# Performance work log

Measured on AMD Instinct MI355X. Metric: run time of the kernel, lower is better.

Reference implementation:

```python
import jax, jax.numpy as jnp
import numpy as np

N_DIM = 512
HEADS = 8
NUM_EXPERTS = 65536
NUM_KEYS = 256      # sqrt(NUM_EXPERTS)
DIM_KEY = 256       # N_DIM // 2
TOPK = 16           # num_experts_per_head (also product_key_topk)
SCALE = 0.02


def setup_inputs() -> dict:
    key = jax.random.key(0)
    k0, k1, k2, k3, k4 = jax.random.split(key, 5)
    x = jax.random.normal(k0, (1, 2048, N_DIM), dtype=jnp.float32)
    W_q = jax.random.normal(k1, (N_DIM, 2 * HEADS * DIM_KEY), dtype=jnp.float32) * SCALE
    keys = jax.random.normal(k2, (HEADS, NUM_KEYS, 2, DIM_KEY), dtype=jnp.float32) * SCALE
    down_embed = jax.random.normal(k3, (NUM_EXPERTS, N_DIM), dtype=jnp.float32) * SCALE
    up_embed = jax.random.normal(k4, (NUM_EXPERTS, N_DIM), dtype=jnp.float32) * SCALE
    return {"x": x, "W_q": W_q, "keys": keys, "down_embed": down_embed, "up_embed": up_embed}


def reference(x, W_q, keys, down_embed, up_embed):
    b, n, d = x.shape
    # queries: [b,n,2*h*dk] -> [2,b,n,h,dk]
    q = (x @ W_q).reshape(b, n, 2, HEADS, DIM_KEY).transpose(2, 0, 1, 3, 4)
    # similarity against product keys: [2,b,n,h,num_keys]
    sim = jnp.einsum('pbnhd,hkpd->pbnhk', q, keys)
    sx, ix = jax.lax.top_k(sim[0], TOPK)   # [b,n,h,TOPK]
    sy, iy = jax.lax.top_k(sim[1], TOPK)
    # cartesian product of the two top-k sets -> [b,n,h,TOPK*TOPK]
    all_scores = (sx[..., :, None] + sy[..., None, :]).reshape(b, n, HEADS, TOPK * TOPK)
    scores, pk_idx = jax.lax.top_k(all_scores, TOPK)  # [b,n,h,TOPK]
    # NOTE: original module indexes embeddings with pk_idx (flat top-k positions),
    # reproduced faithfully here.
    w_down = down_embed[pk_idx]  # [b,n,h,TOPK,d]
    w_up = up_embed[pk_idx]      # [b,n,h,TOPK,d]
    h = jnp.einsum('bnd,bnhkd->bnhk', x, w_down)
    h = jax.nn.gelu(h, approximate=False)
    h = jax.nn.softmax(scores, axis=-1) * h
    return jnp.einsum('bnhk,bnhkd->bnd', h, w_up)
```

## Files before the change

kernel.cpp:

```cpp
#include <hip/hip_runtime.h>
#include <math.h>

#define N_TOK 2048
#define NDIM 512
#define HEADS 8
#define TOPK 16
#define QCOLS 4096
#define LSC 4096.0f
#define ILSC (1.0f/4096.0f)

typedef __attribute__((ext_vector_type(8))) _Float16 f16x8;
typedef __attribute__((ext_vector_type(4))) float f32x4;

__device__ __forceinline__ unsigned short f32_to_f16(float f) {
    _Float16 h = (_Float16)f;
    return __builtin_bit_cast(unsigned short, h);
}
__device__ __forceinline__ float f16_to_f32(unsigned short u) {
    return (float)__builtin_bit_cast(_Float16, u);
}
__device__ __forceinline__ void gl_lds16(const void* g, void* l) {
    __builtin_amdgcn_global_load_lds(
        (const __attribute__((address_space(1))) void*)g,
        (__attribute__((address_space(3))) void*)l, 16, 0, 0);
}

__device__ __forceinline__ void split_f4(const float* __restrict__ src,
                                         unsigned short* __restrict__ dh,
                                         unsigned short* __restrict__ dl,
                                         int i) {
    float4 v = reinterpret_cast<const float4*>(src)[i];
    float vv[4] = {v.x, v.y, v.z, v.w};
    ushort4 h, lo;
    unsigned short* hp = &h.x; unsigned short* lp = &lo.x;
    #pragma unroll
    for (int q = 0; q < 4; ++q) {
        unsigned short hh = f32_to_f16(vv[q]);
        hp[q] = hh;
        lp[q] = f32_to_f16((vv[q] - f16_to_f32(hh)) * LSC);
    }
    reinterpret_cast<ushort4*>(dh)[i] = h;
    reinterpret_cast<ushort4*>(dl)[i] = lo;
}

__global__ __launch_bounds__(256) void kP_split(const float* __restrict__ x,
                                                const float* __restrict__ Wq,
                                                const float* __restrict__ keys,
                                                const float* __restrict__ down,
                                                const float* __restrict__ up,
                                                unsigned short* __restrict__ xh,
                                                unsigned short* __restrict__ xl,
                                                unsigned short* __restrict__ Wqh,
                                                unsigned short* __restrict__ Wql,
                                                unsigned short* __restrict__ ksh,
                                                unsigned short* __restrict__ ksl,
                                                unsigned short* __restrict__ Mth,
                                                unsigned short* __restrict__ Mtl,
                                                unsigned short* __restrict__ upTh,
                                                unsigned short* __restrict__ upTl) {
    const int bid = blockIdx.x;
    const int tid = threadIdx.x;
    if (bid < 256) {
        #pragma unroll
        for (int t = 0; t < 4; ++t) split_f4(x, xh, xl, bid * 1024 + t * 256 + tid);
        return;
    }
    if (bid < 768) {
        const int b = bid - 256;
        #pragma unroll
        for (int t = 0; t < 4; ++t) split_f4(Wq, Wqh, Wql, b * 1024 + t * 256 + tid);
        return;
    }
    if (bid < 1024) {
        const int b = bid - 768;
        #pragma unroll
        for (int t = 0; t < 4; ++t) split_f4(keys, ksh, ksl, b * 1024 + t * 256 + tid);
        return;
    }
    if (bid < 1280) {
        const int e = bid - 1024;
        const int d0 = tid * 2;
        float2 v = *reinterpret_cast<const float2*>(&down[(size_t)e * NDIM + d0]);
        ushort2 h, lo;
        unsigned short h0 = f32_to_f16(v.x);
        unsigned short h1 = f32_to_f16(v.y);
        h.x = h0; h.y = h1;
        lo.x = f32_to_f16((v.x - f16_to_f32(h0)) * LSC);
        lo.y = f32_to_f16((v.y - f16_to_f32(h1)) * LSC);
        *reinterpret_cast<ushort2*>(&Mth[(size_t)(QCOLS + e) * NDIM + d0]) = h;
        *reinterpret_cast<ushort2*>(&Mtl[(size_t)(QCOLS + e) * NDIM + d0]) = lo;
        return;
    }
    const int b = bid - 1280;
    #pragma unroll
    for (int dd = 0; dd < 8; ++dd) {
        const int d = b * 8 + dd;
        const int e = tid;
        const float v = up[(size_t)e * NDIM + d];
        unsigned short hh = f32_to_f16(v);
        upTh[(size_t)d * 256 + e] = hh;
        upTl[(size_t)d * 256 + e] = f32_to_f16((v - f16_to_f32(hh)) * LSC);
    }
}

__global__ __launch_bounds__(256) void kQ_m1(const unsigned short* __restrict__ Wqh,
                                             const unsigned short* __restrict__ Wql,
                                             const unsigned short* __restrict__ ksh,
                                             const unsigned short* __restrict__ ksl,
                                             unsigned short* __restrict__ Mth,
                                             unsigned short* __restrict__ Mtl) {
    __shared__ __align__(16) char lds[36864];
    const int tid = threadIdx.x;
    const int w = tid >> 6, l = tid & 63;
    const int c0 = blockIdx.x * 32;
    const int ph = blockIdx.y;
    const int p = ph >> 3, h = ph & 7;
    const int off = p * 2048 + h * 256;
    f32x4 acch[2][4] = {};
    f32x4 accl[2][4] = {};

    for (int s = 0; s < 8; ++s) {
        const int kk = s * 32;
        __syncthreads();
        {
            const int q = w * 1024 + l * 16;
            const int r = q >> 7;
            const int bsw = (q & 127) ^ ((r & 7) << 4);
            const unsigned short* src = (bsw < 64)
                ? Wqh + (size_t)(c0 + r) * QCOLS + off + kk + (bsw >> 1)
                : Wql + (size_t)(c0 + r) * QCOLS + off + kk + ((bsw - 64) >> 1);
            gl_lds16(src, lds + w * 1024);
        }
        #pragma unroll
        for (int t = 0; t < 8; ++t) {
            const int q = w * 8192 + t * 1024 + l * 16;
            const int r = q >> 7;
            const int bsw = (q & 127) ^ ((r & 7) << 4);
            const unsigned short* src = (bsw < 64)
                ? ksh + ((size_t)(h * 256 + r) * 2 + p) * 256 + kk + (bsw >> 1)
                : ksl + ((size_t)(h * 256 + r) * 2 + p) * 256 + kk + ((bsw - 64) >> 1);
            gl_lds16(src, lds + 4096 + w * 8192 + t * 1024);
        }
        __syncthreads();
        const int bq = (l >> 4) * 16;
        f16x8 ah[2], al[2];
        #pragma unroll
        for (int mi = 0; mi < 2; ++mi) {
            const int ra = mi * 16 + (l & 15);
            const int swz = (ra & 7) << 4;
            ah[mi] = *(const f16x8*)(lds + ra * 128 + (bq ^ swz));
            al[mi] = *(const f16x8*)(lds + ra * 128 + ((bq + 64) ^ swz));
        }
        __builtin_amdgcn_s_setprio(1);
        #pragma unroll
        for (int nj = 0; nj < 4; ++nj) {
            const int rb = w * 64 + nj * 16 + (l & 15);
            const int swz = (rb & 7) << 4;
            f16x8 bh = *(const f16x8*)(lds + 4096 + rb * 128 + (bq ^ swz));
            f16x8 bl = *(const f16x8*)(lds + 4096 + rb * 128 + ((bq + 64) ^ swz));
            #pragma unroll
            for (int mi = 0; mi < 2; ++mi) {
                acch[mi][nj] = __builtin_amdgcn_mfma_f32_16x16x32_f16(ah[mi], bh, acch[mi][nj], 0, 0, 0);
                accl[mi][nj] = __builtin_amdgcn_mfma_f32_16x16x32_f16(ah[mi], bl, accl[mi][nj], 0, 0, 0);
                accl[mi][nj] = __builtin_amdgcn_mfma_f32_16x16x32_f16(al[mi], bh, accl[mi][nj], 0, 0, 0);
            }
        }
        __builtin_amdgcn_s_setprio(0);
    }
    #pragma unroll
    for (int mi = 0; mi < 2; ++mi)
        #pragma unroll
        for (int nj = 0; nj < 4; ++nj) {
            const int k = w * 64 + nj * 16 + (l & 15);
            const int cb = c0 + mi * 16 + (l >> 4) * 4;
            ushort4 h4, l4;
            unsigned short* hp = &h4.x; unsigned short* lp = &l4.x;
            #pragma unroll
            for (int r = 0; r < 4; ++r) {
                const float v = fmaf(accl[mi][nj][r], ILSC, acch[mi][nj][r]);
                unsigned short hh = f32_to_f16(v);
                hp[r] = hh;
                lp[r] = f32_to_f16((v - f16_to_f32(hh)) * LSC);
            }
            *reinterpret_cast<ushort4*>(&Mth[(size_t)(off + k) * NDIM + cb]) = h4;
            *reinterpret_cast<ushort4*>(&Mtl[(size_t)(off + k) * NDIM + cb]) = l4;
        }
}

#define BM 128
#define BN 128
#define BK 32
#define KFBUF 32768
__global__ __launch_bounds__(256, 2) void kF_gemm(const unsigned short* __restrict__ xh,
                                                  const unsigned short* __restrict__ xl,
                                                  const unsigned short* __restrict__ Mth,
                                                  const unsigned short* __restrict__ Mtl,
                                                  float* __restrict__ T,
                                                  float* __restrict__ D) {
    __shared__ __align__(16) char lds[2 * KFBUF];
    const int tid = threadIdx.x;
    const int w = tid >> 6, l = tid & 63;
    const int row0 = blockIdx.x * BM;
    const int by = blockIdx.y;
    const int colbase = by * 128;
    f32x4 acch[8][2] = {};
    f32x4 accl[8][2] = {};

    auto stage = [&](int buf, int s) {
        const int kk = s * BK;
        char* base = lds + buf * KFBUF;
        #pragma unroll
        for (int t = 0; t < 4; ++t) {
            const int q = w * 4096 + t * 1024 + l * 16;
            const int r = q >> 7;
            const int bsw = (q & 127) ^ ((r & 7) << 4);
            const unsigned short* src = (bsw < 64)
                ? xh + (size_t)(row0 + r) * NDIM + kk + (bsw >> 1)
                : xl + (size_t)(row0 + r) * NDIM + kk + ((bsw - 64) >> 1);
            gl_lds16(src, base + w * 4096 + t * 1024);
        }
        #pragma unroll
        for (int t = 0; t < 4; ++t) {
            const int q = w * 4096 + t * 1024 + l * 16;
            const int r = q >> 7;
            const int bsw = (q & 127) ^ ((r & 7) << 4);
            const unsigned short* src = (bsw < 64)
                ? Mth + (size_t)(colbase + r) * NDIM + kk + (bsw >> 1)
                : Mtl + (size_t)(colbase + r) * NDIM + kk + ((bsw - 64) >> 1);
            gl_lds16(src, base + 16384 + w * 4096 + t * 1024);
        }
    };

    stage(0, 0);
    __syncthreads();
    for (int s = 0; s < 16; ++s) {
        if (s + 1 < 16) stage((s + 1) & 1, s + 1);
        const char* base = lds + (s & 1) * KFBUF;
        const int bq = (l >> 4) * 16;
        f16x8 bh[2], bl[2];
        #pragma unroll
        for (int nj = 0; nj < 2; ++nj) {
            const int rb = w * 32 + nj * 16 + (l & 15);
            const int swz = (rb & 7) << 4;
            bh[nj] = *(const f16x8*)(base + 16384 + rb * 128 + (bq ^ swz));
            bl[nj] = *(const f16x8*)(base + 16384 + rb * 128 + ((bq + 64) ^ swz));
        }
        __builtin_amdgcn_s_setprio(1);
        #pragma unroll
        for (int mi = 0; mi < 8; ++mi) {
            const int ra = mi * 16 + (l & 15);
            const int swz = (ra & 7) << 4;
            f16x8 ah = *(const f16x8*)(base + ra * 128 + (bq ^ swz));
            f16x8 al = *(const f16x8*)(base + ra * 128 + ((bq + 64) ^ swz));
            #pragma unroll
            for (int nj = 0; nj < 2; ++nj) {
                acch[mi][nj] = __builtin_amdgcn_mfma_f32_16x16x32_f16(ah, bh[nj], acch[mi][nj], 0, 0, 0);
                accl[mi][nj] = __builtin_amdgcn_mfma_f32_16x16x32_f16(ah, bl[nj], accl[mi][nj], 0, 0, 0);
                accl[mi][nj] = __builtin_amdgcn_mfma_f32_16x16x32_f16(al, bh[nj], accl[mi][nj], 0, 0, 0);
            }
        }
        __builtin_amdgcn_s_setprio(0);
        __syncthreads();
    }

    if (by >= 32) {
        #pragma unroll
        for (int mi = 0; mi < 8; ++mi)
            #pragma unroll
            for (int nj = 0; nj < 2; ++nj)
                #pragma unroll
                for (int r = 0; r < 4; ++r) {
                    const int row = row0 + mi * 16 + (l >> 4) * 4 + r;
                    const int col = (by - 32) * 128 + w * 32 + nj * 16 + (l & 15);
                    D[(size_t)row * 256 + col] = fmaf(accl[mi][nj][r], ILSC, acch[mi][nj][r]);
                }
        return;
    }

    float* Cl = (float*)lds;
    const int grp8 = tid >> 3;
    const int lam8 = tid & 7;
    for (int c = 0; c < 4; ++c) {
        #pragma unroll
        for (int mm = 0; mm < 2; ++mm) {
            const int mi = c * 2 + mm;
            #pragma unroll
            for (int nj = 0; nj < 2; ++nj)
                #pragma unroll
                for (int r = 0; r < 4; ++r)
                    Cl[(mm * 16 + (l >> 4) * 4 + r) * 136 + w * 32 + nj * 16 + (l & 15)] =
                        fmaf(accl[mi][nj][r], ILSC, acch[mi][nj][r]);
        }
        __syncthreads();
        float v[16];
        #pragma unroll
        for (int j = 0; j < 16; ++j) v[j] = Cl[grp8 * 136 + lam8 + 8 * j];
        #pragma unroll
        for (int k = 2; k <= 16; k <<= 1)
            #pragma unroll
            for (int j = k >> 1; j > 0; j >>= 1)
                #pragma unroll
                for (int i = 0; i < 16; ++i) {
                    const int l2 = i ^ j;
                    if (l2 > i) {
                        const bool asc = ((i & k) == 0);
                        const float lo = fminf(v[i], v[l2]), hi = fmaxf(v[i], v[l2]);
                        v[i] = asc ? lo : hi;
                        v[l2] = asc ? hi : lo;
                    }
                }
        #pragma unroll
        for (int lvl = 1; lvl <= 4; lvl <<= 1) {
            float m[16];
            #pragma unroll
            for (int q = 0; q < 16; ++q)
                m[q] = fmaxf(v[q], __shfl_xor(v[15 - q], lvl));
            #pragma unroll
            for (int j = 8; j > 0; j >>= 1)
                #pragma unroll
                for (int i = 0; i < 16; ++i) {
                    const int l2 = i ^ j;
                    if (l2 > i) {
                        const float lo = fminf(m[i], m[l2]), hi = fmaxf(m[i], m[l2]);
                        m[i] = lo; m[l2] = hi;
                    }
                }
            #pragma unroll
            for (int q = 0; q < 16; ++q) v[q] = m[q];
        }
        const int n = row0 + c * 32 + grp8;
        T[((size_t)n * 32 + by) * 16 + 2 * lam8]     = v[15 - 2 * lam8];
        T[((size_t)n * 32 + by) * 16 + 2 * lam8 + 1] = v[14 - 2 * lam8];
        __syncthreads();
    }
}

__device__ const unsigned short CAND_TBL[32] = {
    0x0100, 0x0302, 0x0504, 0x0706, 0x0908, 0x0B0A, 0x0D0C, 0x0F0E,
    0x1110, 0x1312, 0x1514, 0x1716,
    0x2120, 0x2322, 0x3024, 0x3231, 0x4033, 0x4241,
    0x5150, 0x6160, 0x7170,
    0x9080, 0xB0A0, 0xD0C0, 0xF0E0,
    0xFFFF, 0xFFFF, 0xFFFF, 0xFFFF, 0xFFFF, 0xFFFF, 0xFFFF
};

__device__ __forceinline__ float sel16(const float a[16], int i) {
    float b0 = (i & 1) ? a[1] : a[0];
    float b1 = (i & 1) ? a[3] : a[2];
    float b2 = (i & 1) ? a[5] : a[4];
    float b3 = (i & 1) ? a[7] : a[6];
    float b4 = (i & 1) ? a[9] : a[8];
    float b5 = (i & 1) ? a[11] : a[10];
    float b6 = (i & 1) ? a[13] : a[12];
    float b7 = (i & 1) ? a[15] : a[14];
    float c0 = (i & 2) ? b1 : b0;
    float c1 = (i & 2) ? b3 : b2;
    float c2 = (i & 2) ? b5 : b4;
    float c3 = (i & 2) ? b7 : b6;
    float d0 = (i & 4) ? c1 : c0;
    float d1 = (i & 4) ? c3 : c2;
    return (i & 8) ? d1 : d0;
}

__device__ __forceinline__ void merge_desc16(const float* __restrict__ a,
                                             const float* __restrict__ b,
                                             float out_desc[16]) {
    float m[16];
    #pragma unroll
    for (int q = 0; q < 16; ++q) m[q] = fmaxf(a[q], b[15 - q]);
    #pragma unroll
    for (int k = 2; k <= 16; k <<= 1)
        #pragma unroll
        for (int j = k >> 1; j > 0; j >>= 1)
            #pragma unroll
            for (int i = 0; i < 16; ++i) {
                const int l2 = i ^ j;
                if (l2 > i) {
                    const bool asc = ((i & k) == 0);
                    const float lo = fminf(m[i], m[l2]), hi = fmaxf(m[i], m[l2]);
                    m[i] = asc ? lo : hi;
                    m[l2] = asc ? hi : lo;
                }
            }
    #pragma unroll
    for (int q = 0; q < 16; ++q) out_desc[q] = m[15 - q];
}

__global__ __launch_bounds__(256) void kC_combine(const float* __restrict__ T,
                                                  const float* __restrict__ D,
                                                  unsigned short* __restrict__ Wh,
                                                  unsigned short* __restrict__ Wl) {
    __shared__ unsigned long long ckey[8][50];
    __shared__ float winval[8][16];
    __shared__ int winflat[8][16];
    __shared__ int Wrow[256];

    const int tid = threadIdx.x;
    const int n = blockIdx.x;
    const int h = tid >> 5;
    const int lam = tid & 15;

    Wrow[tid] = 0;

    float a0[16], a1[16], b0v[16], b1v[16];
    const float* t00 = &T[((size_t)n * 32 + 2 * h) * 16];
    const float* t01 = &T[((size_t)n * 32 + 2 * h + 1) * 16];
    const float* t10 = &T[((size_t)n * 32 + 16 + 2 * h) * 16];
    const float* t11 = &T[((size_t)n * 32 + 17 + 2 * h) * 16];
    #pragma unroll
    for (int q = 0; q < 16; ++q) {
        a0[q] = t00[q]; a1[q] = t01[q];
        b0v[q] = t10[q]; b1v[q] = t11[q];
    }
    float sxd[16], syd[16];
    merge_desc16(a0, a1, sxd);
    merge_desc16(b0v, b1v, syd);

    const int lc = tid & 31;
    const unsigned int cw = CAND_TBL[lc];
    unsigned long long mykey[2]; float myval[2]; int myflat[2]; int myrank[2] = {0, 0};
    #pragma unroll
    for (int u = 0; u < 2; ++u) {
        const int fl = (cw >> (8 * u)) & 0xFF;
        const float sv = sel16(sxd, fl >> 4) + sel16(syd, fl & 15);
        const unsigned int uv = __float_as_uint(sv);
        const unsigned int mo = (uv & 0x80000000u) ? ~uv : (uv | 0x80000000u);
        mykey[u] = ((unsigned long long)mo << 8) | (unsigned long long)(255 - fl);
        myval[u] = sv; myflat[u] = fl;
        const int slot = lc * 2 + u;
        if (slot < 50) ckey[h][slot] = mykey[u];
    }
    __syncthreads();
    for (int kk = 0; kk < 50; ++kk) {
        const unsigned long long ok = ckey[h][kk];
        myrank[0] += (ok > mykey[0]) ? 1 : 0;
        myrank[1] += (ok > mykey[1]) ? 1 : 0;
    }
    #pragma unroll
    for (int u = 0; u < 2; ++u)
        if (myrank[u] < 16) { winval[h][myrank[u]] = myval[u]; winflat[h][myrank[u]] = myflat[u]; }
    __syncthreads();

    if (!(tid & 16)) {
        const float sc = winval[h][lam];
        const float m0 = winval[h][0];
        float e = expf(sc - m0);
        float esum = e;
        #pragma unroll
        for (int off = 1; off < 16; off <<= 1) esum += __shfl_xor(esum, off);
        const int fl = winflat[h][lam];
        const float hv = D[(size_t)n * 256 + fl];
        const float gg = 0.5f * hv * (1.0f + erff(hv * 0.70710678118654752f));
        const float wv = (e / esum) * gg;
        atomicAdd(&Wrow[fl], __float2int_rn(wv * 4194304.0f));
    }
    __syncthreads();
    const float wfin = (float)Wrow[tid] * (1.0f / 4194304.0f);
    const unsigned short hh = f32_to_f16(wfin);
    Wh[(size_t)n * 256 + tid] = hh;
    Wl[(size_t)n * 256 + tid] = f32_to_f16((wfin - f16_to_f32(hh)) * LSC);
}

__global__ __launch_bounds__(256) void k5_mfma(const unsigned short* __restrict__ Wh,
                                               const unsigned short* __restrict__ Wl,
                                               const unsigned short* __restrict__ upTh,
                                               const unsigned short* __restrict__ upTl,
                                               float* __restrict__ out) {
    __shared__ __align__(16) char lds[20480];
    const int tid = threadIdx.x;
    const int w = tid >> 6, l = tid & 63;
    const int n0 = blockIdx.x * 32;
    const int d0 = blockIdx.y * 128;
    f32x4 acch[2][2] = {};
    f32x4 accl[2][2] = {};

    for (int s = 0; s < 8; ++s) {
        const int kk = s * 32;
        __syncthreads();
        {
            const int q = w * 1024 + l * 16;
            const int r = q >> 7;
            const int bsw = (q & 127) ^ ((r & 7) << 4);
            const unsigned short* src = (bsw < 64)
                ? Wh + (size_t)(n0 + r) * 256 + kk + (bsw >> 1)
                : Wl + (size_t)(n0 + r) * 256 + kk + ((bsw - 64) >> 1);
            gl_lds16(src, lds + w * 1024);
        }
        #pragma unroll
        for (int t = 0; t < 4; ++t) {
            const int q = w * 4096 + t * 1024 + l * 16;
            const int r = q >> 7;
            const int bsw = (q & 127) ^ ((r & 7) << 4);
            const unsigned short* src = (bsw < 64)
                ? upTh + (size_t)(d0 + r) * 256 + kk + (bsw >> 1)
                : upTl + (size_t)(d0 + r) * 256 + kk + ((bsw - 64) >> 1);
            gl_lds16(src, lds + 4096 + w * 4096 + t * 1024);
        }
        __syncthreads();
        const int bq = (l >> 4) * 16;
        f16x8 ah[2], al[2];
        #pragma unroll
        for (int mi = 0; mi < 2; ++mi) {
            const int ra = mi * 16 + (l & 15);
            const int swz = (ra & 7) << 4;
            ah[mi] = *(const f16x8*)(lds + ra * 128 + (bq ^ swz));
            al[mi] = *(const f16x8*)(lds + ra * 128 + ((bq + 64) ^ swz));
        }
        #pragma unroll
        for (int nj = 0; nj < 2; ++nj) {
            const int rb = w * 32 + nj * 16 + (l & 15);
            const int swz = (rb & 7) << 4;
            f16x8 bh = *(const f16x8*)(lds + 4096 + rb * 128 + (bq ^ swz));
            f16x8 bl = *(const f16x8*)(lds + 4096 + rb * 128 + ((bq + 64) ^ swz));
            #pragma unroll
            for (int mi = 0; mi < 2; ++mi) {
                acch[mi][nj] = __builtin_amdgcn_mfma_f32_16x16x32_f16(ah[mi], bh, acch[mi][nj], 0, 0, 0);
                accl[mi][nj] = __builtin_amdgcn_mfma_f32_16x16x32_f16(ah[mi], bl, accl[mi][nj], 0, 0, 0);
                accl[mi][nj] = __builtin_amdgcn_mfma_f32_16x16x32_f16(al[mi], bh, accl[mi][nj], 0, 0, 0);
            }
        }
    }
    #pragma unroll
    for (int mi = 0; mi < 2; ++mi)
        #pragma unroll
        for (int nj = 0; nj < 2; ++nj)
            #pragma unroll
            for (int r = 0; r < 4; ++r) {
                const int row = n0 + mi * 16 + (l >> 4) * 4 + r;
                const int col = d0 + w * 32 + nj * 16 + (l & 15);
                out[(size_t)row * NDIM + col] = fmaf(accl[mi][nj][r], ILSC, acch[mi][nj][r]);
            }
}

extern "C" void kernel_launch(void* const* d_in, const int* in_sizes, int n_in,
                              void* d_out, int out_size, void* d_ws, size_t ws_size,
                              hipStream_t stream) {
    const float* x    = (const float*)d_in[0];
    const float* Wq   = (const float*)d_in[1];
    const float* keys = (const float*)d_in[2];
    const float* down = (const float*)d_in[3];
    const float* up   = (const float*)d_in[4];
    float* out = (float*)d_out;

    char* ws = (char*)d_ws;
    unsigned short* Mth  = (unsigned short*)(ws);
    unsigned short* Mtl  = (unsigned short*)(ws + 4456448);
    unsigned short* xh   = (unsigned short*)(ws + 8912896);
    unsigned short* xl   = (unsigned short*)(ws + 11010048);
    unsigned short* Wqh  = (unsigned short*)(ws + 13107200);
    unsigned short* Wql  = (unsigned short*)(ws + 17301504);
    unsigned short* ksh  = (unsigned short*)(ws + 21495808);
    unsigned short* ksl  = (unsigned short*)(ws + 23592960);
    unsigned short* upTh = (unsigned short*)(ws + 25690112);
    unsigned short* upTl = (unsigned short*)(ws + 25952256);
    float* T             = (float*)(ws + 26214400);
    float* D             = (float*)(ws + 30408704);
    unsigned short* Wh   = (unsigned short*)(ws + 32505856);
    unsigned short* Wl   = (unsigned short*)(ws + 33554432);

    kP_split<<<1344, 256, 0, stream>>>(x, Wq, keys, down, up,
                                       xh, xl, Wqh, Wql, ksh, ksl, Mth, Mtl, upTh, upTl);
    kQ_m1<<<dim3(16, 16), 256, 0, stream>>>(Wqh, Wql, ksh, ksl, Mth, Mtl);
    kF_gemm<<<dim3(16, 34), 256, 0, stream>>>(xh, xl, Mth, Mtl, T, D);
    kC_combine<<<2048, 256, 0, stream>>>(T, D, Wh, Wl);
    k5_mfma<<<dim3(64, 4), 256, 0, stream>>>(Wh, Wl, upTh, upTl, out);
}
```

Baseline: 95.20 us.

## Split fused GEMM top-k epilogue into separate sim write and sort kernel

The GEMM no longer runs the per-tile bitonic top-16 in its epilogue. It now writes the full similarity matrix (2048x4352 fp32) to workspace, and a new kS_sort kernel computes the per-head top-16 over all 256 keys with a wider shuffle merge. The combine kernel then reads the finished top-16 lists directly instead of merging two partial lists. This shortens the GEMM epilogue and drops its LDS round trips and syncthreads, but adds about 35 MB of global traffic and one extra launch, and the workspace regions are reused through aliasing.

```diff
diff --git a/kernel.cpp b/kernel.cpp
--- a/kernel.cpp
+++ b/kernel.cpp
@@ -6,6 +6,7 @@
 #define HEADS 8
 #define TOPK 16
 #define QCOLS 4096
+#define SCOLS 4352
 #define LSC 4096.0f
 #define ILSC (1.0f/4096.0f)
 
@@ -191,12 +192,11 @@
 #define BN 128
 #define BK 32
 #define KFBUF 32768
-__global__ __launch_bounds__(256, 2) void kF_gemm(const unsigned short* __restrict__ xh,
+__global__ __launch_bounds__(256, 2) void kG_gemm(const unsigned short* __restrict__ xh,
                                                   const unsigned short* __restrict__ xl,
                                                   const unsigned short* __restrict__ Mth,
                                                   const unsigned short* __restrict__ Mtl,
-                                                  float* __restrict__ T,
-                                                  float* __restrict__ D) {
+                                                  float* __restrict__ sim) {
     __shared__ __align__(16) char lds[2 * KFBUF];
     const int tid = threadIdx.x;
     const int w = tid >> 6, l = tid & 63;
@@ -263,76 +263,64 @@
         __syncthreads();
     }
 
-    if (by >= 32) {
-        #pragma unroll
-        for (int mi = 0; mi < 8; ++mi)
-            #pragma unroll
-            for (int nj = 0; nj < 2; ++nj)
-                #pragma unroll
-                for (int r = 0; r < 4; ++r) {
-                    const int row = row0 + mi * 16 + (l >> 4) * 4 + r;
-                    const int col = (by - 32) * 128 + w * 32 + nj * 16 + (l & 15);
-                    D[(size_t)row * 256 + col] = fmaf(accl[mi][nj][r], ILSC, acch[mi][nj][r]);
+    #pragma unroll
+    for (int mi = 0; mi < 8; ++mi)
+        #pragma unroll
+        for (int nj = 0; nj < 2; ++nj)
+            #pragma unroll
+            for (int r = 0; r < 4; ++r) {
+                const int row = row0 + mi * 16 + (l >> 4) * 4 + r;
+                const int col = colbase + w * 32 + nj * 16 + (l & 15);
+                sim[(size_t)row * SCOLS + col] = fmaf(accl[mi][nj][r], ILSC, acch[mi][nj][r]);
+            }
+}
+
+__global__ __launch_bounds__(256) void kS_sort(const float* __restrict__ sim,
+                                               float* __restrict__ T) {
+    const int n = blockIdx.x;
+    const int g = threadIdx.x >> 4;
+    const int lam = threadIdx.x & 15;
+    const float* s = sim + (size_t)n * SCOLS + g * 256 + lam * 16;
+    float v[16];
+    #pragma unroll
+    for (int c = 0; c < 4; ++c) {
+        float4 t = *reinterpret_cast<const float4*>(s + c * 4);
+        v[c * 4 + 0] = t.x; v[c * 4 + 1] = t.y; v[c * 4 + 2] = t.z; v[c * 4 + 3] = t.w;
+    }
+    #pragma unroll
+    for (int k = 2; k <= 16; k <<= 1)
+        #pragma unroll
+        for (int j = k >> 1; j > 0; j >>= 1)
+            #pragma unroll
+            for (int i = 0; i < 16; ++i) {
+                const int l2 = i ^ j;
+                if (l2 > i) {
+                    const bool asc = ((i & k) == 0);
+                    const float lo = fminf(v[i], v[l2]), hi = fmaxf(v[i], v[l2]);
+                    v[i] = asc ? lo : hi;
+                    v[l2] = asc ? hi : lo;
                 }
-        return;
-    }
-
-    float* Cl = (float*)lds;
-    const int grp8 = tid >> 3;
-    const int lam8 = tid & 7;
-    for (int c = 0; c < 4; ++c) {
-        #pragma unroll
-        for (int mm = 0; mm < 2; ++mm) {
-            const int mi = c * 2 + mm;
-            #pragma unroll
-            for (int nj = 0; nj < 2; ++nj)
-                #pragma unroll
-                for (int r = 0; r < 4; ++r)
-                    Cl[(mm * 16 + (l >> 4) * 4 + r) * 136 + w * 32 + nj * 16 + (l & 15)] =
-                        fmaf(accl[mi][nj][r], ILSC, acch[mi][nj][r]);
-        }
-        __syncthreads();
-        float v[16];
-        #pragma unroll
-        for (int j = 0; j < 16; ++j) v[j] = Cl[grp8 * 136 + lam8 + 8 * j];
-        #pragma unroll
-        for (int k = 2; k <= 16; k <<= 1)
-            #pragma unroll
-            for (int j = k >> 1; j > 0; j >>= 1)
-                #pragma unroll
-                for (int i = 0; i < 16; ++i) {
-                    const int l2 = i ^ j;
-                    if (l2 > i) {
-                        const bool asc = ((i & k) == 0);
-                        const float lo = fminf(v[i], v[l2]), hi = fmaxf(v[i], v[l2]);
-                        v[i] = asc ? lo : hi;
-                        v[l2] = asc ? hi : lo;
-                    }
+            }
+    #pragma unroll
+    for (int lvl = 1; lvl <= 8; lvl <<= 1) {
+        float m[16];
+        #pragma unroll
+        for (int q = 0; q < 16; ++q)
+            m[q] = fmaxf(v[q], __shfl_xor(v[15 - q], lvl));
+        #pragma unroll
+        for (int j = 8; j > 0; j >>= 1)
+            #pragma unroll
+            for (int i = 0; i < 16; ++i) {
+                const int l2 = i ^ j;
+                if (l2 > i) {
+                    const float lo = fminf(m[i], m[l2]), hi = fmaxf(m[i], m[l2]);
+                    m[i] = lo; m[l2] = hi;
                 }
-        #pragma unroll
-        for (int lvl = 1; lvl <= 4; lvl <<= 1) {
-            float m[16];
-            #pragma unroll
-            for (int q = 0; q < 16; ++q)
-                m[q] = fmaxf(v[q], __shfl_xor(v[15 - q], lvl));
-            #pragma unroll
-            for (int j = 8; j > 0; j >>= 1)
-                #pragma unroll
-                for (int i = 0; i < 16; ++i) {
-                    const int l2 = i ^ j;
-                    if (l2 > i) {
-                        const float lo = fminf(m[i], m[l2]), hi = fmaxf(m[i], m[l2]);
-                        m[i] = lo; m[l2] = hi;
-                    }
-                }
-            #pragma unroll
-            for (int q = 0; q < 16; ++q) v[q] = m[q];
-        }
-        const int n = row0 + c * 32 + grp8;
-        T[((size_t)n * 32 + by) * 16 + 2 * lam8]     = v[15 - 2 * lam8];
-        T[((size_t)n * 32 + by) * 16 + 2 * lam8 + 1] = v[14 - 2 * lam8];
-        __syncthreads();
-    }
+            }
+        #pragma unroll
+        for (int q = 0; q < 16; ++q) v[q] = m[q];
+    }
+    T[((size_t)n * 16 + g) * 16 + lam] = v[15 - lam];
 }
 
 __device__ const unsigned short CAND_TBL[32] = {
@@ -362,32 +350,8 @@
     return (i & 8) ? d1 : d0;
 }
 
-__device__ __forceinline__ void merge_desc16(const float* __restrict__ a,
-                                             const float* __restrict__ b,
-                                             float out_desc[16]) {
-    float m[16];
-    #pragma unroll
-    for (int q = 0; q < 16; ++q) m[q] = fmaxf(a[q], b[15 - q]);
-    #pragma unroll
-    for (int k = 2; k <= 16; k <<= 1)
-        #pragma unroll
-        for (int j = k >> 1; j > 0; j >>= 1)
-            #pragma unroll
-            for (int i = 0; i < 16; ++i) {
-                const int l2 = i ^ j;
-                if (l2 > i) {
-                    const bool asc = ((i & k) == 0);
-                    const float lo = fminf(m[i], m[l2]), hi = fmaxf(m[i], m[l2]);
-                    m[i] = asc ? lo : hi;
-                    m[l2] = asc ? hi : lo;
-                }
-            }
-    #pragma unroll
-    for (int q = 0; q < 16; ++q) out_desc[q] = m[15 - q];
-}
-
 __global__ __launch_bounds__(256) void kC_combine(const float* __restrict__ T,
-                                                  const float* __restrict__ D,
+                                                  const float* __restrict__ sim,
                                                   unsigned short* __restrict__ Wh,
                                                   unsigned short* __restrict__ Wl) {
     __shared__ unsigned long long ckey[8][50];
@@ -402,19 +366,11 @@
 
     Wrow[tid] = 0;
 
-    float a0[16], a1[16], b0v[16], b1v[16];
-    const float* t00 = &T[((size_t)n * 32 + 2 * h) * 16];
-    const float* t01 = &T[((size_t)n * 32 + 2 * h + 1) * 16];
-    const float* t10 = &T[((size_t)n * 32 + 16 + 2 * h) * 16];
-    const float* t11 = &T[((size_t)n * 32 + 17 + 2 * h) * 16];
-    #pragma unroll
-    for (int q = 0; q < 16; ++q) {
-        a0[q] = t00[q]; a1[q] = t01[q];
-        b0v[q] = t10[q]; b1v[q] = t11[q];
-    }
     float sxd[16], syd[16];
-    merge_desc16(a0, a1, sxd);
-    merge_desc16(b0v, b1v, syd);
+    const float* t0 = &T[((size_t)n * 16 + h) * 16];
+    const float* t1 = &T[((size_t)n * 16 + 8 + h) * 16];
+    #pragma unroll
+    for (int q = 0; q < 16; ++q) { sxd[q] = t0[q]; syd[q] = t1[q]; }
 
     const int lc = tid & 31;
     const unsigned int cw = CAND_TBL[lc];
@@ -449,7 +405,7 @@
         #pragma unroll
         for (int off = 1; off < 16; off <<= 1) esum += __shfl_xor(esum, off);
         const int fl = winflat[h][lam];
-        const float hv = D[(size_t)n * 256 + fl];
+        const float hv = sim[(size_t)n * SCOLS + QCOLS + fl];
         const float gg = 0.5f * hv * (1.0f + erff(hv * 0.70710678118654752f));
         const float wv = (e / esum) * gg;
         atomicAdd(&Wrow[fl], __float2int_rn(wv * 4194304.0f));
@@ -547,21 +503,22 @@
     unsigned short* Mtl  = (unsigned short*)(ws + 4456448);
     unsigned short* xh   = (unsigned short*)(ws + 8912896);
     unsigned short* xl   = (unsigned short*)(ws + 11010048);
-    unsigned short* Wqh  = (unsigned short*)(ws + 13107200);
-    unsigned short* Wql  = (unsigned short*)(ws + 17301504);
-    unsigned short* ksh  = (unsigned short*)(ws + 21495808);
-    unsigned short* ksl  = (unsigned short*)(ws + 23592960);
-    unsigned short* upTh = (unsigned short*)(ws + 25690112);
-    unsigned short* upTl = (unsigned short*)(ws + 25952256);
-    float* T             = (float*)(ws + 26214400);
-    float* D             = (float*)(ws + 30408704);
-    unsigned short* Wh   = (unsigned short*)(ws + 32505856);
-    unsigned short* Wl   = (unsigned short*)(ws + 33554432);
+    unsigned short* upTh = (unsigned short*)(ws + 13107200);
+    unsigned short* upTl = (unsigned short*)(ws + 13369344);
+    unsigned short* Wqh  = (unsigned short*)(ws + 13631488);
+    unsigned short* Wql  = (unsigned short*)(ws + 17825792);
+    unsigned short* ksh  = (unsigned short*)(ws + 22020096);
+    unsigned short* ksl  = (unsigned short*)(ws + 24117248);
+    float* sim           = (float*)(ws + 13631488);
+    float* T             = (float*)(ws);
+    unsigned short* Wh   = (unsigned short*)(ws + 2097152);
+    unsigned short* Wl   = (unsigned short*)(ws + 3145728);
 
     kP_split<<<1344, 256, 0, stream>>>(x, Wq, keys, down, up,
                                        xh, xl, Wqh, Wql, ksh, ksl, Mth, Mtl, upTh, upTl);
     kQ_m1<<<dim3(16, 16), 256, 0, stream>>>(Wqh, Wql, ksh, ksl, Mth, Mtl);
-    kF_gemm<<<dim3(16, 34), 256, 0, stream>>>(xh, xl, Mth, Mtl, T, D);
-    kC_combine<<<2048, 256, 0, stream>>>(T, D, Wh, Wl);
+    kG_gemm<<<dim3(16, 34), 256, 0, stream>>>(xh, xl, Mth, Mtl, sim);
+    kS_sort<<<2048, 256, 0, stream>>>(sim, T);
+    kC_combine<<<2048, 256, 0, stream>>>(T, sim, Wh, Wl);
     k5_mfma<<<dim3(64, 4), 256, 0, stream>>>(Wh, Wl, upTh, upTl, out);
 }
```

New measurement: 103.5 us. 1.09x slower.

## Use 2x2 warp tiling and XCD-aware block swizzle in fused GEMM

Applied to the files above, without the earlier changes.

Changes the per-warp tile in the main GEMM from 128x32 (warps split along N) to 64x64 (a 2x2 warp grid), so each warp reads fewer LDS fragments per MFMA. It also flattens the grid to 1D and remaps block ids so that blocks landing on the same XCD share column tiles, aiming for better L2 reuse. The epilogue is adjusted so only the warps owning each row chunk write to the staging buffer. This adds extra branching in the epilogue, and the remap relies on the 544-block grid dividing evenly by 8.

```diff
diff --git a/kernel.cpp b/kernel.cpp
--- a/kernel.cpp
+++ b/kernel.cpp
@@ -200,11 +200,14 @@
     __shared__ __align__(16) char lds[2 * KFBUF];
     const int tid = threadIdx.x;
     const int w = tid >> 6, l = tid & 63;
-    const int row0 = blockIdx.x * BM;
-    const int by = blockIdx.y;
+    const int wm = w >> 1, wn = w & 1;
+    const int orig = blockIdx.x;
+    const int swz = (orig & 7) * 68 + (orig >> 3);
+    const int by = swz >> 4;
+    const int row0 = (swz & 15) * BM;
     const int colbase = by * 128;
-    f32x4 acch[8][2] = {};
-    f32x4 accl[8][2] = {};
+    f32x4 acch[4][4] = {};
+    f32x4 accl[4][4] = {};
 
     auto stage = [&](int buf, int s) {
         const int kk = s * BK;
@@ -237,23 +240,23 @@
         if (s + 1 < 16) stage((s + 1) & 1, s + 1);
         const char* base = lds + (s & 1) * KFBUF;
         const int bq = (l >> 4) * 16;
-        f16x8 bh[2], bl[2];
-        #pragma unroll
-        for (int nj = 0; nj < 2; ++nj) {
-            const int rb = w * 32 + nj * 16 + (l & 15);
-            const int swz = (rb & 7) << 4;
-            bh[nj] = *(const f16x8*)(base + 16384 + rb * 128 + (bq ^ swz));
-            bl[nj] = *(const f16x8*)(base + 16384 + rb * 128 + ((bq + 64) ^ swz));
+        f16x8 bh[4], bl[4];
+        #pragma unroll
+        for (int nj = 0; nj < 4; ++nj) {
+            const int rb = wn * 64 + nj * 16 + (l & 15);
+            const int sz = (rb & 7) << 4;
+            bh[nj] = *(const f16x8*)(base + 16384 + rb * 128 + (bq ^ sz));
+            bl[nj] = *(const f16x8*)(base + 16384 + rb * 128 + ((bq + 64) ^ sz));
         }
         __builtin_amdgcn_s_setprio(1);
         #pragma unroll
-        for (int mi = 0; mi < 8; ++mi) {
-            const int ra = mi * 16 + (l & 15);
-            const int swz = (ra & 7) << 4;
-            f16x8 ah = *(const f16x8*)(base + ra * 128 + (bq ^ swz));
-            f16x8 al = *(const f16x8*)(base + ra * 128 + ((bq + 64) ^ swz));
-            #pragma unroll
-            for (int nj = 0; nj < 2; ++nj) {
+        for (int mi = 0; mi < 4; ++mi) {
+            const int ra = wm * 64 + mi * 16 + (l & 15);
+            const int sz = (ra & 7) << 4;
+            f16x8 ah = *(const f16x8*)(base + ra * 128 + (bq ^ sz));
+            f16x8 al = *(const f16x8*)(base + ra * 128 + ((bq + 64) ^ sz));
+            #pragma unroll
+            for (int nj = 0; nj < 4; ++nj) {
                 acch[mi][nj] = __builtin_amdgcn_mfma_f32_16x16x32_f16(ah, bh[nj], acch[mi][nj], 0, 0, 0);
                 accl[mi][nj] = __builtin_amdgcn_mfma_f32_16x16x32_f16(ah, bl[nj], accl[mi][nj], 0, 0, 0);
                 accl[mi][nj] = __builtin_amdgcn_mfma_f32_16x16x32_f16(al, bh[nj], accl[mi][nj], 0, 0, 0);
@@ -265,13 +268,13 @@
 
     if (by >= 32) {
         #pragma unroll
-        for (int mi = 0; mi < 8; ++mi)
-            #pragma unroll
-            for (int nj = 0; nj < 2; ++nj)
+        for (int mi = 0; mi < 4; ++mi)
+            #pragma unroll
+            for (int nj = 0; nj < 4; ++nj)
                 #pragma unroll
                 for (int r = 0; r < 4; ++r) {
-                    const int row = row0 + mi * 16 + (l >> 4) * 4 + r;
-                    const int col = (by - 32) * 128 + w * 32 + nj * 16 + (l & 15);
+                    const int row = row0 + wm * 64 + mi * 16 + (l >> 4) * 4 + r;
+                    const int col = (by - 32) * 128 + wn * 64 + nj * 16 + (l & 15);
                     D[(size_t)row * 256 + col] = fmaf(accl[mi][nj][r], ILSC, acch[mi][nj][r]);
                 }
         return;
@@ -281,15 +284,17 @@
     const int grp8 = tid >> 3;
     const int lam8 = tid & 7;
     for (int c = 0; c < 4; ++c) {
-        #pragma unroll
-        for (int mm = 0; mm < 2; ++mm) {
-            const int mi = c * 2 + mm;
-            #pragma unroll
-            for (int nj = 0; nj < 2; ++nj)
+        if (wm == (c >> 1)) {
+            #pragma unroll
+            for (int u = 0; u < 2; ++u) {
+                const int mi = (c & 1) * 2 + u;
                 #pragma unroll
-                for (int r = 0; r < 4; ++r)
-                    Cl[(mm * 16 + (l >> 4) * 4 + r) * 136 + w * 32 + nj * 16 + (l & 15)] =
-                        fmaf(accl[mi][nj][r], ILSC, acch[mi][nj][r]);
+                for (int nj = 0; nj < 4; ++nj)
+                    #pragma unroll
+                    for (int r = 0; r < 4; ++r)
+                        Cl[(u * 16 + (l >> 4) * 4 + r) * 136 + wn * 64 + nj * 16 + (l & 15)] =
+                            fmaf(accl[mi][nj][r], ILSC, acch[mi][nj][r]);
+            }
         }
         __syncthreads();
         float v[16];
@@ -561,7 +566,7 @@
     kP_split<<<1344, 256, 0, stream>>>(x, Wq, keys, down, up,
                                        xh, xl, Wqh, Wql, ksh, ksl, Mth, Mtl, upTh, upTl);
     kQ_m1<<<dim3(16, 16), 256, 0, stream>>>(Wqh, Wql, ksh, ksl, Mth, Mtl);
-    kF_gemm<<<dim3(16, 34), 256, 0, stream>>>(xh, xl, Mth, Mtl, T, D);
+    kF_gemm<<<544, 256, 0, stream>>>(xh, xl, Mth, Mtl, T, D);
     kC_combine<<<2048, 256, 0, stream>>>(T, D, Wh, Wl);
     k5_mfma<<<dim3(64, 4), 256, 0, stream>>>(Wh, Wl, upTh, upTl, out);
 }
```

New measurement: 100.3 us. +5.4%, slower.
